# Optimization experiments

Hardware: AMD Instinct MI355X
Metric: run time of the kernel (lower is better)

## Reference

```python
import jax, jax.numpy as jnp
import numpy as np

N = 100000      # nodes
E = 1600000     # edges (avg degree 16)
D_IN = 128
D_H = 128


def setup_inputs() -> dict:
    key = jax.random.key(0)
    ks = jax.random.split(key, 8)
    s_in = 1.0 / np.sqrt(D_IN)
    s_h = 1.0 / np.sqrt(D_H)
    return {
        "x": jax.random.normal(ks[0], (N, D_IN), dtype=jnp.float32),
        "edge_index": jax.random.randint(ks[1], (2, E), 0, N, dtype=jnp.int32),
        "W0": jax.random.uniform(ks[2], (D_IN, D_H), jnp.float32, -s_in, s_in),
        "b0": jnp.zeros((D_H,), jnp.float32),
        "W1": jax.random.uniform(ks[3], (D_H, D_H), jnp.float32, -s_h, s_h),
        "b1": jnp.zeros((D_H,), jnp.float32),
        "W2": jax.random.uniform(ks[4], (D_H, D_H), jnp.float32, -s_h, s_h),
        "b2": jnp.zeros((D_H,), jnp.float32),
    }


def reference(x, edge_index, W0, b0, W1, b1, W2, b2):
    n = x.shape[0]
    # GCN normalization with self-loops (PyG gcn_norm)
    sl = jnp.arange(n, dtype=edge_index.dtype)
    row = jnp.concatenate([edge_index[0], sl])  # destination
    col = jnp.concatenate([edge_index[1], sl])  # source
    deg = jax.ops.segment_sum(jnp.ones_like(col, jnp.float32), col, num_segments=n)
    dis = jnp.where(deg > 0, jax.lax.rsqrt(jnp.where(deg > 0, deg, 1.0)), 0.0)
    norm = (dis[row] * dis[col])[:, None]  # [E+N, 1]

    def conv(h, W, b):
        h = h @ W                                   # [N, D_H]
        msg = h[col] * norm                         # gather + scale, [E+N, D_H]
        return jax.ops.segment_sum(msg, row, num_segments=n) + b

    h0 = conv(x, W0, b0)
    h1 = conv(jax.nn.relu(h0), W1, b1)
    h2 = conv(jax.nn.relu(h1), W2, b2)
    # x_hidden: [N, num_layers, D_H]
    return jnp.stack([h0, h1, h2], axis=1)
```

## Files before the change

kernel.cpp:

```cpp
#include <hip/hip_runtime.h>

typedef _Float16 half8 __attribute__((ext_vector_type(8)));
typedef _Float16 half4 __attribute__((ext_vector_type(4)));
typedef _Float16 half2v __attribute__((ext_vector_type(2)));
typedef float f4 __attribute__((ext_vector_type(4)));

#define NBK 1024
#define NBLK 128


__global__ __launch_bounds__(256)
void k_bhist(const int* __restrict__ ei, int E, int chunk,
             int* __restrict__ hb) {
  __shared__ int hd[NBK], hs[NBK];
  int t = threadIdx.x, blk = blockIdx.x;
  for (int i = t; i < NBK; i += 256) { hd[i] = 0; hs[i] = 0; }
  __syncthreads();
  int start = blk * chunk, end = min(E, start + chunk);
  for (int i = start + t; i < end; i += 256) {
    int dst = ei[i];
    int src = ei[E + i];
    atomicAdd(&hd[dst >> 8], 1);
    atomicAdd(&hs[src >> 8], 1);
  }
  __syncthreads();
  for (int i = t; i < NBK; i += 256) {
    hb[blk * NBK + i] = hd[i];
    hb[(NBLK + blk) * NBK + i] = hs[i];
  }
}

__global__ void k_colscan(int* __restrict__ hb, int* __restrict__ totals) {
  int tid = blockIdx.x * 256 + threadIdx.x;
  int* tab = hb + (tid >> 10) * (NBLK * NBK);
  int j = tid & (NBK - 1);
  int run = 0;
  for (int b = 0; b < NBLK; ++b) {
    int idx = b * NBK + j;
    int v = tab[idx];
    tab[idx] = run;
    run += v;
  }
  totals[tid] = run;
}

__global__ void k_bscan2(const int* __restrict__ totals, int* __restrict__ boffs,
                         int* __restrict__ soffs, int* __restrict__ offs,
                         int N, int E) {
  __shared__ int s[NBK];
  int t = threadIdx.x;
  int v = totals[t];
  s[t] = v;
  __syncthreads();
  for (int off = 1; off < NBK; off <<= 1) {
    int x = (t >= off) ? s[t - off] : 0;
    __syncthreads();
    s[t] += x;
    __syncthreads();
  }
  boffs[t] = s[t] - v;
  if (t == NBK - 1) boffs[NBK] = s[t];
  __syncthreads();
  int v2 = totals[NBK + t];
  s[t] = v2;
  __syncthreads();
  for (int off = 1; off < NBK; off <<= 1) {
    int x = (t >= off) ? s[t - off] : 0;
    __syncthreads();
    s[t] += x;
    __syncthreads();
  }
  soffs[t] = s[t] - v2;
  if (t == NBK - 1) soffs[NBK] = s[t];
  if (t == 0) offs[N] = E;
}

__global__ __launch_bounds__(256)
void k_bscatter(const int* __restrict__ ei, int E, int chunk,
                const int* __restrict__ hb, const int* __restrict__ boffs,
                const int* __restrict__ soffs,
                unsigned long long* __restrict__ pairs,
                unsigned char* __restrict__ srcb) {
  __shared__ int based[NBK], posd[NBK], bases[NBK], poss[NBK];
  int t = threadIdx.x, blk = blockIdx.x;
  for (int i = t; i < NBK; i += 256) {
    based[i] = hb[blk * NBK + i] + boffs[i];
    posd[i] = 0;
    bases[i] = hb[(NBLK + blk) * NBK + i] + soffs[i];
    poss[i] = 0;
  }
  __syncthreads();
  int start = blk * chunk, end = min(E, start + chunk);
  for (int i = start + t; i < end; i += 256) {
    int dst = ei[i];
    int src = ei[E + i];
    int bd = dst >> 8, bs = src >> 8;
    int p = atomicAdd(&posd[bd], 1);
    pairs[based[bd] + p] =
        ((unsigned long long)(unsigned)src << 32) | (unsigned)dst;
    int q = atomicAdd(&poss[bs], 1);
    srcb[bases[bs] + q] = (unsigned char)(src & 255);
  }
}

__global__ __launch_bounds__(256)
void k_deg(const unsigned char* __restrict__ srcb, const int* __restrict__ soffs,
           float* __restrict__ dis, int N) {
  __shared__ int h[256];
  int b = blockIdx.x, t = threadIdx.x;
  h[t] = 0;
  __syncthreads();
  int lo = soffs[b], hi = soffs[b + 1];
  for (int i = lo + t; i < hi; i += 256) atomicAdd(&h[srcb[i]], 1);
  __syncthreads();
  int v = (b << 8) + t;
  if (v < N) dis[v] = rsqrtf((float)(h[t] + 1));
}

__global__ __launch_bounds__(256)
void k_fscatter(const unsigned long long* __restrict__ pairs,
                const int* __restrict__ boffs,
                int* __restrict__ offs, int* __restrict__ srcs, int N) {
  __shared__ int h[256], sc[256], cur[256];
  int b = blockIdx.x, t = threadIdx.x;
  h[t] = 0;
  __syncthreads();
  int pl = boffs[b], ph = boffs[b + 1];
  for (int i = pl + t; i < ph; i += 256)
    atomicAdd(&h[(int)(pairs[i] & 255ull)], 1);
  __syncthreads();
  sc[t] = h[t];
  __syncthreads();
  for (int off = 1; off < 256; off <<= 1) {
    int x = (t >= off) ? sc[t - off] : 0;
    __syncthreads();
    sc[t] += x;
    __syncthreads();
  }
  int excl = sc[t] - h[t];
  int v = (b << 8) + t;
  if (v < N) offs[v] = pl + excl;
  cur[t] = pl + excl;
  __syncthreads();
  for (int i = pl + t; i < ph; i += 256) {
    unsigned long long pk = pairs[i];
    int p = atomicAdd(&cur[(int)(pk & 255ull)], 1);
    srcs[p] = (int)(unsigned)(pk >> 32);
  }
}

__global__ void k_prepw(const float* __restrict__ W0, const float* __restrict__ W1,
                        const float* __restrict__ W2, _Float16* __restrict__ Wt) {
  int i = blockIdx.x * blockDim.x + threadIdx.x;
  int m = i >> 14;
  int j = i & 16383;
  int c = j >> 7, k = j & 127;
  const float* W = (m == 0) ? W0 : (m == 1) ? W1 : W2;
  Wt[i] = (_Float16)W[k * 128 + c];
}


#define LDH 136

__global__ __launch_bounds__(256, 2)
void k_gemm(const float* __restrict__ in, int in_stride, int do_relu,
            const _Float16* __restrict__ Wt_g, const float* __restrict__ dis,
            _Float16* __restrict__ hws, int N) {
  __shared__ _Float16 Wt[128 * LDH];
  int t = threadIdx.x;
  int rbase = blockIdx.x * 128;

#pragma unroll
  for (int i = 0; i < 8; ++i) {
    int s = t + i * 256;
    int c = s >> 4, kh = s & 15;
    half8 w = ((const half8*)Wt_g)[s];
    *(half8*)&Wt[c * LDH + kh * 8] = w;
  }
  __syncthreads();

  int wv = t >> 6, lane = t & 63;
  int r0 = wv * 32;
  int lr = lane & 15, lg = lane >> 4;

  f4 acc[2][8];
#pragma unroll
  for (int fm = 0; fm < 2; ++fm)
#pragma unroll
    for (int fn = 0; fn < 8; ++fn) acc[fm][fn] = (f4){0.f, 0.f, 0.f, 0.f};

#pragma unroll
  for (int ks = 0; ks < 4; ++ks) {
    int k0 = ks * 32 + lg * 8;
    half8 a[8];
#pragma unroll
    for (int fn = 0; fn < 8; ++fn)
      a[fn] = *(const half8*)&Wt[(fn * 16 + lr) * LDH + k0];
#pragma unroll
    for (int fm = 0; fm < 2; ++fm) {
      int gr = rbase + r0 + fm * 16 + lr;
      float4 v0 = make_float4(0.f, 0.f, 0.f, 0.f);
      float4 v1 = make_float4(0.f, 0.f, 0.f, 0.f);
      if (gr < N) {
        const float* pr = in + (size_t)gr * in_stride + k0;
        v0 = *(const float4*)pr;
        v1 = *(const float4*)(pr + 4);
      }
      if (do_relu) {
        v0.x = fmaxf(v0.x, 0.f); v0.y = fmaxf(v0.y, 0.f);
        v0.z = fmaxf(v0.z, 0.f); v0.w = fmaxf(v0.w, 0.f);
        v1.x = fmaxf(v1.x, 0.f); v1.y = fmaxf(v1.y, 0.f);
        v1.z = fmaxf(v1.z, 0.f); v1.w = fmaxf(v1.w, 0.f);
      }
      half8 b;
      b[0] = (_Float16)v0.x; b[1] = (_Float16)v0.y;
      b[2] = (_Float16)v0.z; b[3] = (_Float16)v0.w;
      b[4] = (_Float16)v1.x; b[5] = (_Float16)v1.y;
      b[6] = (_Float16)v1.z; b[7] = (_Float16)v1.w;
#pragma unroll
      for (int fn = 0; fn < 8; ++fn)
        acc[fm][fn] = __builtin_amdgcn_mfma_f32_16x16x32_f16(a[fn], b, acc[fm][fn], 0, 0, 0);
    }
  }

#pragma unroll
  for (int fm = 0; fm < 2; ++fm) {
    int gr = rbase + r0 + fm * 16 + lr;
    if (gr >= N) continue;
    float dv = dis[gr];
#pragma unroll
    for (int fn = 0; fn < 8; ++fn) {
      f4 d = acc[fm][fn];
      half4 hv;
      hv[0] = (_Float16)(d[0] * dv);
      hv[1] = (_Float16)(d[1] * dv);
      hv[2] = (_Float16)(d[2] * dv);
      hv[3] = (_Float16)(d[3] * dv);
      *(half4*)(hws + (size_t)gr * 128 + fn * 16 + lg * 4) = hv;
    }
  }
}


__global__ __launch_bounds__(256)
void k_agg(const _Float16* __restrict__ hws, const int* __restrict__ offs,
           const int* __restrict__ srcs, const float* __restrict__ dis,
           const float* __restrict__ bias, float* __restrict__ out,
           int N, int layer) {
  int wv = threadIdx.x >> 6, lane = threadIdx.x & 63;
  int v = blockIdx.x * 4 + wv;
  if (v >= N) return;

  const uint* h32 = (const uint*)hws;
  uint hv = h32[(size_t)v * 64 + lane];
  half2v h = __builtin_bit_cast(half2v, hv);
  float ax = (float)h[0], ay = (float)h[1];

  int e0 = offs[v], e1 = offs[v + 1];
  int e = e0;
  for (; e + 8 <= e1; e += 8) {
    int s0 = srcs[e + 0], s1 = srcs[e + 1], s2 = srcs[e + 2], s3 = srcs[e + 3];
    int s4 = srcs[e + 4], s5 = srcs[e + 5], s6 = srcs[e + 6], s7 = srcs[e + 7];
    uint u0 = h32[(size_t)s0 * 64 + lane];
    uint u1 = h32[(size_t)s1 * 64 + lane];
    uint u2 = h32[(size_t)s2 * 64 + lane];
    uint u3 = h32[(size_t)s3 * 64 + lane];
    uint u4 = h32[(size_t)s4 * 64 + lane];
    uint u5 = h32[(size_t)s5 * 64 + lane];
    uint u6 = h32[(size_t)s6 * 64 + lane];
    uint u7 = h32[(size_t)s7 * 64 + lane];
    half2v p0 = __builtin_bit_cast(half2v, u0);
    half2v p1 = __builtin_bit_cast(half2v, u1);
    half2v p2 = __builtin_bit_cast(half2v, u2);
    half2v p3 = __builtin_bit_cast(half2v, u3);
    half2v p4 = __builtin_bit_cast(half2v, u4);
    half2v p5 = __builtin_bit_cast(half2v, u5);
    half2v p6 = __builtin_bit_cast(half2v, u6);
    half2v p7 = __builtin_bit_cast(half2v, u7);
    ax += (float)p0[0] + (float)p1[0] + (float)p2[0] + (float)p3[0]
        + (float)p4[0] + (float)p5[0] + (float)p6[0] + (float)p7[0];
    ay += (float)p0[1] + (float)p1[1] + (float)p2[1] + (float)p3[1]
        + (float)p4[1] + (float)p5[1] + (float)p6[1] + (float)p7[1];
  }
  for (; e < e1; ++e) {
    int s = srcs[e];
    uint u = h32[(size_t)s * 64 + lane];
    half2v p = __builtin_bit_cast(half2v, u);
    ax += (float)p[0];
    ay += (float)p[1];
  }

  float dv = dis[v];
  float2 b = ((const float2*)bias)[lane];
  float2 o;
  o.x = fmaf(dv, ax, b.x);
  o.y = fmaf(dv, ay, b.y);
  *(float2*)(out + (size_t)v * 384 + layer * 128 + 2 * lane) = o;
}


extern "C" void kernel_launch(void* const* d_in, const int* in_sizes, int n_in,
                              void* d_out, int out_size, void* d_ws, size_t ws_size,
                              hipStream_t stream) {
  const float* x  = (const float*)d_in[0];
  const int*   ei = (const int*)d_in[1];
  const float* W0 = (const float*)d_in[2];
  const float* b0 = (const float*)d_in[3];
  const float* W1 = (const float*)d_in[4];
  const float* b1 = (const float*)d_in[5];
  const float* W2 = (const float*)d_in[6];
  const float* b2 = (const float*)d_in[7];
  float* out = (float*)d_out;

  int N = in_sizes[0] / 128;
  int E = in_sizes[1] / 2;
  int nb = (N + 255) >> 8;
  int chunk = (((E + NBLK - 1) / NBLK) + 255) & ~255;

  char* p = (char*)d_ws;
  auto alloc = [&](size_t sz) { char* r = p; p += (sz + 255) & ~(size_t)255; return r; };
  _Float16* hws  = (_Float16*)alloc((size_t)N * 128 * 2);
  float* dis     = (float*)alloc((size_t)N * 4);
  int*   offs    = (int*)alloc((size_t)(N + 1) * 4);
  int*   srcs    = (int*)alloc((size_t)E * 4);
  _Float16* Wt   = (_Float16*)alloc((size_t)3 * 128 * 128 * 2);
  int*   hb      = (int*)alloc((size_t)2 * NBLK * NBK * 4);
  int*   totals  = (int*)alloc((size_t)2 * NBK * 4);
  int*   boffs   = (int*)alloc((size_t)(NBK + 1) * 4);
  int*   soffs   = (int*)alloc((size_t)(NBK + 1) * 4);
  unsigned long long* pairs = (unsigned long long*)alloc((size_t)E * 8);
  unsigned char* srcb = (unsigned char*)alloc((size_t)E);

  k_bhist<<<NBLK, 256, 0, stream>>>(ei, E, chunk, hb);
  k_colscan<<<8, 256, 0, stream>>>(hb, totals);
  k_bscan2<<<1, 1024, 0, stream>>>(totals, boffs, soffs, offs, N, E);
  k_bscatter<<<NBLK, 256, 0, stream>>>(ei, E, chunk, hb, boffs, soffs, pairs, srcb);
  k_deg<<<nb, 256, 0, stream>>>(srcb, soffs, dis, N);
  k_fscatter<<<nb, 256, 0, stream>>>(pairs, boffs, offs, srcs, N);
  k_prepw<<<192, 256, 0, stream>>>(W0, W1, W2, Wt);

  int gG = (N + 127) / 128;
  int gA = (N + 3) / 4;

  k_gemm<<<gG, 256, 0, stream>>>(x, 128, 0, Wt, dis, hws, N);
  k_agg<<<gA, 256, 0, stream>>>(hws, offs, srcs, dis, b0, out, N, 0);
  k_gemm<<<gG, 256, 0, stream>>>(out, 384, 1, Wt + 16384, dis, hws, N);
  k_agg<<<gA, 256, 0, stream>>>(hws, offs, srcs, dis, b1, out, N, 1);
  k_gemm<<<gG, 256, 0, stream>>>(out + 128, 384, 1, Wt + 32768, dis, hws, N);
  k_agg<<<gA, 256, 0, stream>>>(hws, offs, srcs, dis, b2, out, N, 2);
}
```

Baseline: 385.2 us.

## Slice hidden features into column panels and aggregate per-XCD slice with work stealing

The GEMM now writes the fp16 hidden matrix as eight 16-column panels instead of row-major rows. The aggregation kernel becomes persistent. Each block reads its XCC id, starts on the panel matching its XCD, and pulls 256-node chunks from per-panel atomic counters. Each thread owns one node and gathers 32-byte panel rows from neighbours. The intent is to keep each panel's working set (N*32 bytes) resident in one XCD's L2, so neighbour gathers hit cache instead of HBM. The cost is one thread per node with serial edge loops, divergence from uneven degrees, uncoalesced 64-byte output writes, and extra barriers around the atomics.

```diff
diff --git a/kernel.cpp b/kernel.cpp
--- a/kernel.cpp
+++ b/kernel.cpp
@@ -2,7 +2,6 @@
 
 typedef _Float16 half8 __attribute__((ext_vector_type(8)));
 typedef _Float16 half4 __attribute__((ext_vector_type(4)));
-typedef _Float16 half2v __attribute__((ext_vector_type(2)));
 typedef float f4 __attribute__((ext_vector_type(4)));
 
 #define NBK 1024
@@ -46,9 +45,10 @@
 
 __global__ void k_bscan2(const int* __restrict__ totals, int* __restrict__ boffs,
                          int* __restrict__ soffs, int* __restrict__ offs,
-                         int N, int E) {
+                         int* __restrict__ ctrs, int N, int E) {
   __shared__ int s[NBK];
   int t = threadIdx.x;
+  if (t < 24) ctrs[t] = 0;
   int v = totals[t];
   s[t] = v;
   __syncthreads();
@@ -169,6 +169,7 @@
   __shared__ _Float16 Wt[128 * LDH];
   int t = threadIdx.x;
   int rbase = blockIdx.x * 128;
+  size_t slst = (size_t)N * 16;
 
 #pragma unroll
   for (int i = 0; i < 8; ++i) {
@@ -236,66 +237,93 @@
       hv[1] = (_Float16)(d[1] * dv);
       hv[2] = (_Float16)(d[2] * dv);
       hv[3] = (_Float16)(d[3] * dv);
-      *(half4*)(hws + (size_t)gr * 128 + fn * 16 + lg * 4) = hv;
+      *(half4*)(hws + (size_t)fn * slst + (size_t)gr * 16 + lg * 4) = hv;
     }
   }
 }
 
-
-__global__ __launch_bounds__(256)
-void k_agg(const _Float16* __restrict__ hws, const int* __restrict__ offs,
-           const int* __restrict__ srcs, const float* __restrict__ dis,
-           const float* __restrict__ bias, float* __restrict__ out,
-           int N, int layer) {
-  int wv = threadIdx.x >> 6, lane = threadIdx.x & 63;
-  int v = blockIdx.x * 4 + wv;
-  if (v >= N) return;
-
-  const uint* h32 = (const uint*)hws;
-  uint hv = h32[(size_t)v * 64 + lane];
-  half2v h = __builtin_bit_cast(half2v, hv);
-  float ax = (float)h[0], ay = (float)h[1];
-
-  int e0 = offs[v], e1 = offs[v + 1];
-  int e = e0;
-  for (; e + 8 <= e1; e += 8) {
-    int s0 = srcs[e + 0], s1 = srcs[e + 1], s2 = srcs[e + 2], s3 = srcs[e + 3];
-    int s4 = srcs[e + 4], s5 = srcs[e + 5], s6 = srcs[e + 6], s7 = srcs[e + 7];
-    uint u0 = h32[(size_t)s0 * 64 + lane];
-    uint u1 = h32[(size_t)s1 * 64 + lane];
-    uint u2 = h32[(size_t)s2 * 64 + lane];
-    uint u3 = h32[(size_t)s3 * 64 + lane];
-    uint u4 = h32[(size_t)s4 * 64 + lane];
-    uint u5 = h32[(size_t)s5 * 64 + lane];
-    uint u6 = h32[(size_t)s6 * 64 + lane];
-    uint u7 = h32[(size_t)s7 * 64 + lane];
-    half2v p0 = __builtin_bit_cast(half2v, u0);
-    half2v p1 = __builtin_bit_cast(half2v, u1);
-    half2v p2 = __builtin_bit_cast(half2v, u2);
-    half2v p3 = __builtin_bit_cast(half2v, u3);
-    half2v p4 = __builtin_bit_cast(half2v, u4);
-    half2v p5 = __builtin_bit_cast(half2v, u5);
-    half2v p6 = __builtin_bit_cast(half2v, u6);
-    half2v p7 = __builtin_bit_cast(half2v, u7);
-    ax += (float)p0[0] + (float)p1[0] + (float)p2[0] + (float)p3[0]
-        + (float)p4[0] + (float)p5[0] + (float)p6[0] + (float)p7[0];
-    ay += (float)p0[1] + (float)p1[1] + (float)p2[1] + (float)p3[1]
-        + (float)p4[1] + (float)p5[1] + (float)p6[1] + (float)p7[1];
-  }
-  for (; e < e1; ++e) {
-    int s = srcs[e];
-    uint u = h32[(size_t)s * 64 + lane];
-    half2v p = __builtin_bit_cast(half2v, u);
-    ax += (float)p[0];
-    ay += (float)p[1];
-  }
-
-  float dv = dis[v];
-  float2 b = ((const float2*)bias)[lane];
-  float2 o;
-  o.x = fmaf(dv, ax, b.x);
-  o.y = fmaf(dv, ay, b.y);
-  *(float2*)(out + (size_t)v * 384 + layer * 128 + 2 * lane) = o;
+#define AGG_CHUNK 256
+
+__global__ __launch_bounds__(256)
+void k_agg2(const _Float16* __restrict__ hws, const int* __restrict__ offs,
+            const int* __restrict__ srcs, const float* __restrict__ dis,
+            const float* __restrict__ bias, float* __restrict__ out,
+            int N, int layer, int* __restrict__ ctr) {
+  __shared__ int scur;
+  int t = threadIdx.x;
+  int myx;
+  asm volatile("s_getreg_b32 %0, hwreg(HW_REG_XCC_ID)" : "=s"(myx));
+  myx &= 7;
+  int nchunks = (N + AGG_CHUNK - 1) / AGG_CHUNK;
+  size_t slst = (size_t)N * 16;
+
+  for (int rr = 0; rr < 8; ++rr) {
+    int sl = (myx + rr) & 7;
+    const _Float16* hsl = hws + (size_t)sl * slst;
+    int f0 = sl * 16;
+    for (;;) {
+      if (t == 0) scur = atomicAdd(&ctr[sl], 1);
+      __syncthreads();
+      int c = scur;
+      __syncthreads();
+      if (c >= nchunks) break;
+      int v = c * AGG_CHUNK + t;
+      if (v >= N) continue;
+
+      const half8* vp = (const half8*)(hsl + (size_t)v * 16);
+      half8 a0 = vp[0], a1 = vp[1];
+      float acc[16];
+#pragma unroll
+      for (int i = 0; i < 8; ++i) { acc[i] = (float)a0[i]; acc[8 + i] = (float)a1[i]; }
+
+      int e0 = __builtin_nontemporal_load(&offs[v]);
+      int e1 = __builtin_nontemporal_load(&offs[v + 1]);
+      int e = e0;
+      for (; e + 4 <= e1; e += 4) {
+        int s0 = __builtin_nontemporal_load(&srcs[e + 0]);
+        int s1 = __builtin_nontemporal_load(&srcs[e + 1]);
+        int s2 = __builtin_nontemporal_load(&srcs[e + 2]);
+        int s3 = __builtin_nontemporal_load(&srcs[e + 3]);
+        const half8* p0 = (const half8*)(hsl + (size_t)s0 * 16);
+        const half8* p1 = (const half8*)(hsl + (size_t)s1 * 16);
+        const half8* p2 = (const half8*)(hsl + (size_t)s2 * 16);
+        const half8* p3 = (const half8*)(hsl + (size_t)s3 * 16);
+        half8 x0 = p0[0], y0 = p0[1];
+        half8 x1 = p1[0], y1 = p1[1];
+        half8 x2 = p2[0], y2 = p2[1];
+        half8 x3 = p3[0], y3 = p3[1];
+#pragma unroll
+        for (int i = 0; i < 8; ++i) {
+          acc[i]     += (float)x0[i] + (float)x1[i] + (float)x2[i] + (float)x3[i];
+          acc[8 + i] += (float)y0[i] + (float)y1[i] + (float)y2[i] + (float)y3[i];
+        }
+      }
+      for (; e < e1; ++e) {
+        int s = __builtin_nontemporal_load(&srcs[e]);
+        const half8* ps = (const half8*)(hsl + (size_t)s * 16);
+        half8 x = ps[0], y = ps[1];
+#pragma unroll
+        for (int i = 0; i < 8; ++i) {
+          acc[i] += (float)x[i];
+          acc[8 + i] += (float)y[i];
+        }
+      }
+
+      float dv = dis[v];
+      const f4* bp = (const f4*)(bias + f0);
+      f4* op = (f4*)(out + (size_t)v * 384 + layer * 128 + f0);
+#pragma unroll
+      for (int q = 0; q < 4; ++q) {
+        f4 bb = bp[q];
+        f4 oo;
+        oo[0] = fmaf(dv, acc[q * 4 + 0], bb[0]);
+        oo[1] = fmaf(dv, acc[q * 4 + 1], bb[1]);
+        oo[2] = fmaf(dv, acc[q * 4 + 2], bb[2]);
+        oo[3] = fmaf(dv, acc[q * 4 + 3], bb[3]);
+        __builtin_nontemporal_store(oo, op + q);
+      }
+    }
+  }
 }
 
 
@@ -330,22 +358,22 @@
   int*   soffs   = (int*)alloc((size_t)(NBK + 1) * 4);
   unsigned long long* pairs = (unsigned long long*)alloc((size_t)E * 8);
   unsigned char* srcb = (unsigned char*)alloc((size_t)E);
+  int*   ctrs    = (int*)alloc(24 * 4);
 
   k_bhist<<<NBLK, 256, 0, stream>>>(ei, E, chunk, hb);
   k_colscan<<<8, 256, 0, stream>>>(hb, totals);
-  k_bscan2<<<1, 1024, 0, stream>>>(totals, boffs, soffs, offs, N, E);
+  k_bscan2<<<1, 1024, 0, stream>>>(totals, boffs, soffs, offs, ctrs, N, E);
   k_bscatter<<<NBLK, 256, 0, stream>>>(ei, E, chunk, hb, boffs, soffs, pairs, srcb);
   k_deg<<<nb, 256, 0, stream>>>(srcb, soffs, dis, N);
   k_fscatter<<<nb, 256, 0, stream>>>(pairs, boffs, offs, srcs, N);
   k_prepw<<<192, 256, 0, stream>>>(W0, W1, W2, Wt);
 
   int gG = (N + 127) / 128;
-  int gA = (N + 3) / 4;
 
   k_gemm<<<gG, 256, 0, stream>>>(x, 128, 0, Wt, dis, hws, N);
-  k_agg<<<gA, 256, 0, stream>>>(hws, offs, srcs, dis, b0, out, N, 0);
+  k_agg2<<<2048, 256, 0, stream>>>(hws, offs, srcs, dis, b0, out, N, 0, ctrs);
   k_gemm<<<gG, 256, 0, stream>>>(out, 384, 1, Wt + 16384, dis, hws, N);
-  k_agg<<<gA, 256, 0, stream>>>(hws, offs, srcs, dis, b1, out, N, 1);
+  k_agg2<<<2048, 256, 0, stream>>>(hws, offs, srcs, dis, b1, out, N, 1, ctrs + 8);
   k_gemm<<<gG, 256, 0, stream>>>(out + 128, 384, 1, Wt + 32768, dis, hws, N);
-  k_agg<<<gA, 256, 0, stream>>>(hws, offs, srcs, dis, b2, out, N, 2);
-}
+  k_agg2<<<2048, 256, 0, stream>>>(hws, offs, srcs, dis, b2, out, N, 2, ctrs + 16);
+}
```

After: 1.138 ms. 2.95x slower.

## Slice hidden features into 16-column planes and aggregate per slice

Applied to the files above, without the earlier changes.

The GEMM now writes the fp16 hidden matrix as eight column-slabs of 16 features each (N x 16 per slab) instead of row-major N x 128. Aggregation is split so that each block handles one slab for a chunk of 256 nodes. Each wave processes one node, with eight lane groups each gathering a different neighbor's 32-byte slice, followed by a shuffle reduction. The aim is to shrink each slab's working set so gathers hit in L2/MALL, at the cost of 32-byte scattered loads, repeated reads of offsets and sources across slices, and an extra cross-lane reduction.

```diff
diff --git a/kernel.cpp b/kernel.cpp
--- a/kernel.cpp
+++ b/kernel.cpp
@@ -4,6 +4,7 @@
 typedef _Float16 half4 __attribute__((ext_vector_type(4)));
 typedef _Float16 half2v __attribute__((ext_vector_type(2)));
 typedef float f4 __attribute__((ext_vector_type(4)));
+typedef float f2 __attribute__((ext_vector_type(2)));
 
 #define NBK 1024
 #define NBLK 128
@@ -169,6 +170,7 @@
   __shared__ _Float16 Wt[128 * LDH];
   int t = threadIdx.x;
   int rbase = blockIdx.x * 128;
+  size_t slst = (size_t)N * 16;
 
 #pragma unroll
   for (int i = 0; i < 8; ++i) {
@@ -236,66 +238,54 @@
       hv[1] = (_Float16)(d[1] * dv);
       hv[2] = (_Float16)(d[2] * dv);
       hv[3] = (_Float16)(d[3] * dv);
-      *(half4*)(hws + (size_t)gr * 128 + fn * 16 + lg * 4) = hv;
-    }
-  }
-}
-
-
-__global__ __launch_bounds__(256)
-void k_agg(const _Float16* __restrict__ hws, const int* __restrict__ offs,
-           const int* __restrict__ srcs, const float* __restrict__ dis,
-           const float* __restrict__ bias, float* __restrict__ out,
-           int N, int layer) {
+      *(half4*)(hws + (size_t)fn * slst + (size_t)gr * 16 + lg * 4) = hv;
+    }
+  }
+}
+
+#define AGG_NPB 256
+
+__global__ __launch_bounds__(256)
+void k_agg3(const _Float16* __restrict__ hws, const int* __restrict__ offs,
+            const int* __restrict__ srcs, const float* __restrict__ dis,
+            const float* __restrict__ bias, float* __restrict__ out,
+            int N, int layer) {
+  int sl = blockIdx.x & 7;
+  int chunkId = blockIdx.x >> 3;
   int wv = threadIdx.x >> 6, lane = threadIdx.x & 63;
-  int v = blockIdx.x * 4 + wv;
-  if (v >= N) return;
-
-  const uint* h32 = (const uint*)hws;
-  uint hv = h32[(size_t)v * 64 + lane];
-  half2v h = __builtin_bit_cast(half2v, hv);
-  float ax = (float)h[0], ay = (float)h[1];
-
-  int e0 = offs[v], e1 = offs[v + 1];
-  int e = e0;
-  for (; e + 8 <= e1; e += 8) {
-    int s0 = srcs[e + 0], s1 = srcs[e + 1], s2 = srcs[e + 2], s3 = srcs[e + 3];
-    int s4 = srcs[e + 4], s5 = srcs[e + 5], s6 = srcs[e + 6], s7 = srcs[e + 7];
-    uint u0 = h32[(size_t)s0 * 64 + lane];
-    uint u1 = h32[(size_t)s1 * 64 + lane];
-    uint u2 = h32[(size_t)s2 * 64 + lane];
-    uint u3 = h32[(size_t)s3 * 64 + lane];
-    uint u4 = h32[(size_t)s4 * 64 + lane];
-    uint u5 = h32[(size_t)s5 * 64 + lane];
-    uint u6 = h32[(size_t)s6 * 64 + lane];
-    uint u7 = h32[(size_t)s7 * 64 + lane];
-    half2v p0 = __builtin_bit_cast(half2v, u0);
-    half2v p1 = __builtin_bit_cast(half2v, u1);
-    half2v p2 = __builtin_bit_cast(half2v, u2);
-    half2v p3 = __builtin_bit_cast(half2v, u3);
-    half2v p4 = __builtin_bit_cast(half2v, u4);
-    half2v p5 = __builtin_bit_cast(half2v, u5);
-    half2v p6 = __builtin_bit_cast(half2v, u6);
-    half2v p7 = __builtin_bit_cast(half2v, u7);
-    ax += (float)p0[0] + (float)p1[0] + (float)p2[0] + (float)p3[0]
-        + (float)p4[0] + (float)p5[0] + (float)p6[0] + (float)p7[0];
-    ay += (float)p0[1] + (float)p1[1] + (float)p2[1] + (float)p3[1]
-        + (float)p4[1] + (float)p5[1] + (float)p6[1] + (float)p7[1];
-  }
-  for (; e < e1; ++e) {
-    int s = srcs[e];
-    uint u = h32[(size_t)s * 64 + lane];
-    half2v p = __builtin_bit_cast(half2v, u);
-    ax += (float)p[0];
-    ay += (float)p[1];
-  }
-
-  float dv = dis[v];
-  float2 b = ((const float2*)bias)[lane];
-  float2 o;
-  o.x = fmaf(dv, ax, b.x);
-  o.y = fmaf(dv, ay, b.y);
-  *(float2*)(out + (size_t)v * 384 + layer * 128 + 2 * lane) = o;
+  int fp = lane & 7;
+  int g  = lane >> 3;
+  size_t slst = (size_t)N * 16;
+  const _Float16* hsl = hws + (size_t)sl * slst;
+  int f0 = sl * 16;
+  f2 bb = *(const f2*)(bias + f0 + fp * 2);
+
+  int vend = min(N, chunkId * AGG_NPB + AGG_NPB);
+  for (int v = chunkId * AGG_NPB + wv; v < vend; v += 4) {
+    int e0 = __builtin_nontemporal_load(&offs[v]);
+    int e1 = __builtin_nontemporal_load(&offs[v + 1]);
+    int cnt = e1 - e0 + 1;
+    float ax = 0.f, ay = 0.f;
+    for (int it = g; it < cnt; it += 8) {
+      int s = (it == 0) ? v : __builtin_nontemporal_load(&srcs[e0 + it - 1]);
+      uint u = *(const uint*)(hsl + (size_t)s * 16 + fp * 2);
+      half2v h = __builtin_bit_cast(half2v, u);
+      ax += (float)h[0];
+      ay += (float)h[1];
+    }
+#pragma unroll
+    for (int off = 8; off < 64; off <<= 1) {
+      ax += __shfl_xor(ax, off);
+      ay += __shfl_xor(ay, off);
+    }
+    if (g == 0) {
+      float dv = dis[v];
+      f2 o;
+      o[0] = fmaf(dv, ax, bb[0]);
+      o[1] = fmaf(dv, ay, bb[1]);
+      __builtin_nontemporal_store(o, (f2*)(out + (size_t)v * 384 + layer * 128 + f0 + fp * 2));
+    }
+  }
 }
 
 
@@ -340,12 +330,12 @@
   k_prepw<<<192, 256, 0, stream>>>(W0, W1, W2, Wt);
 
   int gG = (N + 127) / 128;
-  int gA = (N + 3) / 4;
+  int gA = 8 * ((N + AGG_NPB - 1) / AGG_NPB);
 
   k_gemm<<<gG, 256, 0, stream>>>(x, 128, 0, Wt, dis, hws, N);
-  k_agg<<<gA, 256, 0, stream>>>(hws, offs, srcs, dis, b0, out, N, 0);
+  k_agg3<<<gA, 256, 0, stream>>>(hws, offs, srcs, dis, b0, out, N, 0);
   k_gemm<<<gG, 256, 0, stream>>>(out, 384, 1, Wt + 16384, dis, hws, N);
-  k_agg<<<gA, 256, 0, stream>>>(hws, offs, srcs, dis, b1, out, N, 1);
+  k_agg3<<<gA, 256, 0, stream>>>(hws, offs, srcs, dis, b1, out, N, 1);
   k_gemm<<<gG, 256, 0, stream>>>(out + 128, 384, 1, Wt + 32768, dis, hws, N);
-  k_agg<<<gA, 256, 0, stream>>>(hws, offs, srcs, dis, b2, out, N, 2);
-}
+  k_agg3<<<gA, 256, 0, stream>>>(hws, offs, srcs, dis, b2, out, N, 2);
+}
```

Result: slower. 1.199 ms (+211.3%).
